# Kernel tuning notes

Measured on AMD Instinct MI355X. Metric: run time of the kernel, lower is better.

The kernel has to match this reference:

```python
import jax, jax.numpy as jnp
import numpy as np

DEPTH = 10
NUM_LEAVES = 2 ** DEPTH  # 1024


def setup_inputs() -> dict:
    key = jax.random.key(0)
    k1, k2, k3, k4 = jax.random.split(key, 4)
    B, C, T = 4096, 512, 4096
    x = jax.random.normal(k1, (B, C), dtype=jnp.float32)
    # thresholds = 6*rand - 3, as in __init__
    thresholds = 6.0 * jax.random.uniform(k2, (T, NUM_LEAVES - 1), dtype=jnp.float32) - 3.0
    ordinals = jax.random.randint(k3, (T, NUM_LEAVES - 1), 0, C, dtype=jnp.int32)
    weights = jax.random.normal(k4, (T, NUM_LEAVES), dtype=jnp.float32)
    return {"x": x, "thresholds": thresholds, "ordinals": ordinals, "weights": weights}


def reference(x, thresholds, ordinals, weights):
    """Random hinge forest forward.

    For each sample b and tree t: traverse the perfect binary tree of depth
    DEPTH.  At node n, margin m = x[b, ordinals[t, n]] - thresholds[t, n];
    go right (child 2n+2) if m > 0 else left (child 2n+1).  Track the signed
    margin of minimum magnitude along the path.  Output is
    |min-margin| * weights[t, leaf].
    """
    B = x.shape[0]
    T = thresholds.shape[0]
    tr = jnp.arange(T)  # [T], broadcasts against [B, T] node indices
    node = jnp.zeros((B, T), dtype=jnp.int32)
    minm = jnp.full((B, T), jnp.inf, dtype=x.dtype)
    for _ in range(DEPTH):
        thr = thresholds[tr, node]                      # [B, T]
        ordv = ordinals[tr, node]                       # [B, T] feature ids
        feat = jnp.take_along_axis(x, ordv, axis=1)     # [B, T]
        m = feat - thr
        minm = jnp.where(jnp.abs(m) < jnp.abs(minm), m, minm)
        node = 2 * node + 1 + (m > 0).astype(jnp.int32)
    leaf = node - (NUM_LEAVES - 1)                      # [B, T] in [0, 2^depth)
    w = weights[tr, leaf]                               # [B, T]
    return jnp.abs(minm) * w
```

## Files before the change

kernel.cpp:

```cpp
#include <hip/hip_runtime.h>
#include <hip/hip_fp16.h>

#define BB 4096
#define CC 512
#define TT 4096
#define NN 1023
#define NL 1024
#define DEPTH 10


__device__ __forceinline__ unsigned pack_node(float th, int o) {
    return ((unsigned)o << 16) | (unsigned)__half_as_ushort(__float2half(th));
}

__global__ __launch_bounds__(256)
void pack_trees(const float* __restrict__ thr, const int* __restrict__ ord,
                const float* __restrict__ wts,
                unsigned* __restrict__ pk_lo, uint4* __restrict__ tails) {
    int t = blockIdx.x, tid = threadIdx.x;
    const float* tr = thr + (size_t)t * NN;
    const int*   oo = ord + (size_t)t * NN;
    unsigned* plo = pk_lo + ((size_t)t << 9);
    #pragma unroll
    for (int k = 0; k < 2; ++k) {
        int j = k * 256 + tid;
        plo[j] = (j == 0) ? 0u : pack_node(tr[j - 1], oo[j - 1]);
    }
    int i = tid;
    int nL = 511 + 2 * i, nR = 512 + 2 * i;
    unsigned ndL = pack_node(tr[nL], oo[nL]);
    unsigned ndR = pack_node(tr[nR], oo[nR]);
    float4 w4 = *(const float4*)(wts + ((size_t)t << 10) + 4 * i);
    unsigned w01 = (unsigned)__half_as_ushort(__float2half(w4.x)) |
                   ((unsigned)__half_as_ushort(__float2half(w4.y)) << 16);
    unsigned w23 = (unsigned)__half_as_ushort(__float2half(w4.z)) |
                   ((unsigned)__half_as_ushort(__float2half(w4.w)) << 16);
    tails[((size_t)t << 8) + i] = make_uint4(ndL, ndR, w01, w23);
}

__global__ __launch_bounds__(256)
void pack_x16(const float* __restrict__ x, unsigned short* __restrict__ xt16) {
    __shared__ float tile[64][65];
    int tx = threadIdx.x & 63, ty = threadIdx.x >> 6;
    int b0 = blockIdx.x * 64;
    int c0 = blockIdx.y * 64;
    #pragma unroll
    for (int i = 0; i < 16; ++i) {
        int rr = i * 4 + ty;
        tile[rr][tx] = x[(size_t)(b0 + rr) * CC + c0 + tx];
    }
    __syncthreads();
    #pragma unroll
    for (int i = 0; i < 16; ++i) {
        int cr = i * 4 + ty;
        xt16[(size_t)(c0 + cr) * BB + b0 + tx] =
            __half_as_ushort(__float2half(tile[tx][cr]));
    }
}

#define LDS_BYTES 163840

typedef __attribute__((address_space(1))) const void gv_t;
typedef __attribute__((address_space(3))) void lv_t;

__global__ __launch_bounds__(1024, 1)
void rhf_main(const unsigned* __restrict__ pk_lo, const uint4* __restrict__ tails,
              const unsigned short* __restrict__ xt16, float* __restrict__ out) {
    extern __shared__ char smem[];
    unsigned short* xs16 = (unsigned short*)smem;
    unsigned*       trl  = (unsigned*)(smem + 65536);
    float*          res  = (float*)(smem + 131072);

    const int tid  = threadIdx.x;
    const int lane = tid & 63;
    const int wv   = tid >> 6;
    const int bi   = blockIdx.x;
    const int tb    = ((bi & 7) << 2) + ((bi >> 3) >> 6);
    const int panel = (bi >> 3) & 63;

    const char* gsrc0 = (const char*)pk_lo + ((size_t)(tb * 128) << 11);
    char* ldst = (char*)trl + wv * 4096 + lane * 16;
    auto dma = [&](int g) {
        const char* s = gsrc0 + ((size_t)(g * 32 + wv * 2) << 11) + lane * 16;
        #pragma unroll
        for (int q = 0; q < 4; ++q)
            __builtin_amdgcn_global_load_lds((gv_t*)(s + q * 1024),
                                             (lv_t*)(ldst + q * 1024), 16, 0, 0);
    };

    dma(0);

    {
        const unsigned short* src = xt16 + (size_t)panel * 64;
        #pragma unroll
        for (int k = 0; k < 4; ++k) {
            int i4 = k * 1024 + tid;
            int c  = i4 >> 3;
            int o8 = (i4 & 7) << 3;
            uint4 v = *(const uint4*)(src + (size_t)c * BB + o8);
            *(uint4*)(xs16 + ((size_t)i4 << 3)) = v;
        }
    }
    __syncthreads();

    #pragma unroll 1
    for (int g = 0; g < 4; ++g) {
        if (g > 0) {
            asm volatile("s_waitcnt vmcnt(0)" ::: "memory");
            __builtin_amdgcn_sched_barrier(0);
        }
        const int t0 = tb * 128 + g * 32 + wv * 2;
        const unsigned* pkw = trl + wv * 1024;

        float amin[2]; int sl[2]; unsigned nd[2]; uint4 rec[2];
        #pragma unroll
        for (int c = 0; c < 2; ++c) {
            amin[c] = __builtin_inff(); sl[c] = 1; nd[c] = pkw[c * 512 + 1];
        }

        #pragma unroll
        for (int d = 0; d < 9; ++d) {
            uint2 ch[2];
            #pragma unroll
            for (int c = 0; c < 2; ++c) {
                if (d < 8) ch[c] = *(const uint2*)(pkw + c * 512 + 2 * sl[c]);
                else       rec[c] = tails[((size_t)(t0 + c) << 8) + (sl[c] - 256)];
            }
            #pragma unroll
            for (int c = 0; c < 2; ++c) {
                float thv = __half2float(__ushort_as_half((unsigned short)(nd[c] & 0xffffu)));
                int   orv = (int)(nd[c] >> 16);
                float feat = __half2float(__ushort_as_half(xs16[(orv << 6) + lane]));
                float m = feat - thv;
                amin[c] = fminf(amin[c], fabsf(m));
                int right = (m > 0.0f) ? 1 : 0;
                sl[c] = 2 * sl[c] + right;
                if (d < 8) nd[c] = right ? ch[c].y : ch[c].x;
            }
        }

        if (g < 3) { dma(g + 1); __builtin_amdgcn_sched_barrier(0); }

        #pragma unroll
        for (int c = 0; c < 2; ++c) {
            int right8 = sl[c] & 1;
            unsigned nd9 = right8 ? rec[c].y : rec[c].x;
            float thv = __half2float(__ushort_as_half((unsigned short)(nd9 & 0xffffu)));
            int   orv = (int)(nd9 >> 16);
            float feat = __half2float(__ushort_as_half(xs16[(orv << 6) + lane]));
            float m = feat - thv;
            amin[c] = fminf(amin[c], fabsf(m));
            int right9 = (m > 0.0f) ? 1 : 0;
            unsigned wsel = right8 ? rec[c].w : rec[c].z;
            unsigned short wb = (unsigned short)(right9 ? (wsel >> 16) : (wsel & 0xffffu));
            float w = __half2float(__ushort_as_half(wb));
            int col = g * 32 + wv * 2 + c;
            res[(lane << 7) + ((col + lane) & 127)] = amin[c] * w;
        }
    }
    __syncthreads();

    float* obase = out + (size_t)(tb * 128);
    #pragma unroll
    for (int k = 0; k < 8; ++k) {
        int idx = k * 1024 + tid;
        int rr = idx >> 7, cc = idx & 127;
        float v = res[(rr << 7) + ((cc + rr) & 127)];
        obase[((size_t)panel * 64 + rr) * TT + cc] = v;
    }
}

#define F_SP 32
#define F_TG 16
#define F_GROUPS 8
#define F_TPB (F_TG * F_GROUPS)
#define F_NPANELS (BB / F_SP)
#define F_LDS 147456

__global__ __launch_bounds__(512, 1)
void rhf_fallback(const float* __restrict__ x, const float* __restrict__ thr_g,
                  const int* __restrict__ ord_g, const float* __restrict__ wts,
                  float* __restrict__ out) {
    extern __shared__ char smem[];
    float*        xs  = (float*)(smem);
    unsigned int* pk  = (unsigned int*)(smem + 65536);
    float*        res = (float*)(smem + 131072);
    const int tid = threadIdx.x, s = tid & 31, slot = tid >> 5;
    const int panel = blockIdx.x & (F_NPANELS - 1), tb = blockIdx.x >> 7;
    const float* xbase = x + (size_t)panel * F_SP * CC;
    #pragma unroll
    for (int k = 0; k < (F_SP * CC) / 512; ++k) {
        int idx = k * 512 + tid, r = idx >> 9, c = idx & 511;
        xs[(c << 5) + r] = xbase[r * CC + c];
    }
    float4 pthr[8]; int4 pord[8]; float tthr[3]; int tord[3];
    auto prefetch = [&](int g) {
        const size_t base = (size_t)(tb * F_TPB + g * F_TG + slot) * NN;
        #pragma unroll
        for (int k = 0; k < 8; ++k) {
            int j = k * 128 + 4 * s;
            if (j < 1020) { pthr[k] = *(const float4*)(thr_g + base + j);
                            pord[k] = *(const int4*)(ord_g + base + j); }
            else { tthr[0]=thr_g[base+1020]; tord[0]=ord_g[base+1020];
                   tthr[1]=thr_g[base+1021]; tord[1]=ord_g[base+1021];
                   tthr[2]=thr_g[base+1022]; tord[2]=ord_g[base+1022]; }
        }
    };
    auto pack1 = [](float f, int o) -> unsigned int {
        return ((unsigned int)o << 16) | (unsigned int)__half_as_ushort(__float2half(f));
    };
    auto commit = [&]() {
        unsigned int* pt = pk + (slot << 10);
        #pragma unroll
        for (int k = 0; k < 8; ++k) {
            int j = k * 128 + 4 * s;
            if (j < 1020) {
                pt[1+j+0]=pack1(pthr[k].x,pord[k].x); pt[1+j+1]=pack1(pthr[k].y,pord[k].y);
                pt[1+j+2]=pack1(pthr[k].z,pord[k].z); pt[1+j+3]=pack1(pthr[k].w,pord[k].w);
            } else { pt[1+1020]=pack1(tthr[0],tord[0]); pt[1+1021]=pack1(tthr[1],tord[1]);
                     pt[1+1022]=pack1(tthr[2],tord[2]); }
        }
    };
    prefetch(0);
    __builtin_amdgcn_sched_barrier(0);
    for (int g = 0; g < F_GROUPS; ++g) {
        __syncthreads();
        commit();
        __syncthreads();
        if (g + 1 < F_GROUPS) prefetch(g + 1);
        __builtin_amdgcn_sched_barrier(0);
        const int t = tb * F_TPB + g * F_TG + slot;
        const unsigned int* pkt = pk + (slot << 10);
        float minm = __builtin_inff();
        int sl = 1;
        unsigned int cur = pkt[1];
        #pragma unroll
        for (int d = 0; d < DEPTH; ++d) {
            uint2 ch;
            if (d < DEPTH - 1) ch = *(const uint2*)(pkt + 2 * sl);
            float thv = __half2float(__ushort_as_half((unsigned short)(cur & 0xffffu)));
            int orv = (int)(cur >> 16);
            float feat = xs[(orv << 5) + s];
            float m = feat - thv;
            bool take = fabsf(m) < fabsf(minm);
            minm = take ? m : minm;
            int right = (m > 0.0f) ? 1 : 0;
            sl = 2 * sl + right;
            if (d < DEPTH - 1) cur = right ? ch.y : ch.x;
        }
        int leaf = sl - NL;
        float w = wts[(size_t)t * NL + leaf];
        int col = g * F_TG + slot;
        res[(s << 7) + ((col + s) & 127)] = fabsf(minm) * w;
    }
    __syncthreads();
    float* obase = out + (size_t)panel * F_SP * TT + (size_t)tb * F_TPB;
    #pragma unroll
    for (int k = 0; k < (F_SP * F_TPB) / 512; ++k) {
        int idx = k * 512 + tid, rr = idx >> 7, c = idx & 127;
        obase[(size_t)rr * TT + c] = res[(rr << 7) + ((c + rr) & 127)];
    }
}

extern "C" void kernel_launch(void* const* d_in, const int* in_sizes, int n_in,
                              void* d_out, int out_size, void* d_ws, size_t ws_size,
                              hipStream_t stream) {
    const float* x    = (const float*)d_in[0];
    const float* thr  = (const float*)d_in[1];
    const int*   ordv = (const int*)d_in[2];
    const float* wts  = (const float*)d_in[3];
    float*       out  = (float*)d_out;

    const size_t pk_bytes   = (size_t)TT * 512 * 4;
    const size_t tail_bytes = (size_t)TT * 256 * 16;
    const size_t xt_bytes   = (size_t)CC * BB * 2;

    if (d_ws && ws_size >= pk_bytes + tail_bytes + xt_bytes) {
        unsigned*       pk_lo = (unsigned*)d_ws;
        uint4*          tails = (uint4*)((char*)d_ws + pk_bytes);
        unsigned short* xt16  = (unsigned short*)((char*)d_ws + pk_bytes + tail_bytes);
        pack_trees<<<TT, 256, 0, stream>>>(thr, ordv, wts, pk_lo, tails);
        dim3 gx(BB / 64, CC / 64);
        pack_x16<<<gx, 256, 0, stream>>>(x, xt16);
        hipFuncSetAttribute((const void*)rhf_main,
                            hipFuncAttributeMaxDynamicSharedMemorySize, LDS_BYTES);
        rhf_main<<<2048, 1024, LDS_BYTES, stream>>>(pk_lo, tails, xt16, out);
    } else {
        hipFuncSetAttribute((const void*)rhf_fallback,
                            hipFuncAttributeMaxDynamicSharedMemorySize, F_LDS);
        rhf_fallback<<<F_NPANELS * (TT / F_TPB), 512, F_LDS, stream>>>(x, thr, ordv, wts, out);
    }
}
```

Before: 114.5 us.

## Use packed fp16 margin math and prefetch tail records one level earlier

The per-node margin computation for the two trees each wave handles now runs as one packed f16x2 subtract. The running minimum is kept as a packed u16 min on the sign-cleared bits, replacing separate fp32 converts, subtracts and mins. The global tail-record loads are issued at depth 7 and fetch both candidate records, so their latency overlaps two traversal levels instead of one. The costs are twice the tail load traffic, and margins and the right/left decision now computed in fp16 rather than fp32, which can change rounding near zero and the minimum-magnitude value.

```diff
diff --git a/kernel.cpp b/kernel.cpp
--- a/kernel.cpp
+++ b/kernel.cpp
@@ -58,6 +58,29 @@
     }
 }
 
+typedef unsigned short u16x2 __attribute__((ext_vector_type(2)));
+
+static __device__ __forceinline__ unsigned psub_f16x2(unsigned a, unsigned b) {
+    __half2 ah, bh;
+    __builtin_memcpy(&ah, &a, 4);
+    __builtin_memcpy(&bh, &b, 4);
+    __half2 r = ah - bh;
+    unsigned u; __builtin_memcpy(&u, &r, 4); return u;
+}
+static __device__ __forceinline__ unsigned pmin_u16x2(unsigned a, unsigned b) {
+    u16x2 av, bv;
+    __builtin_memcpy(&av, &a, 4);
+    __builtin_memcpy(&bv, &b, 4);
+    u16x2 m = __builtin_elementwise_min(av, bv);
+    unsigned u; __builtin_memcpy(&u, &m, 4); return u;
+}
+static __device__ __forceinline__ float f16lo_to_f32(unsigned u) {
+    return __half2float(__ushort_as_half((unsigned short)(u & 0xffffu)));
+}
+static __device__ __forceinline__ float f16hi_to_f32(unsigned u) {
+    return __half2float(__ushort_as_half((unsigned short)(u >> 16)));
+}
+
 #define LDS_BYTES 163840
 
 typedef __attribute__((address_space(1))) const void gv_t;
@@ -112,51 +135,74 @@
         const int t0 = tb * 128 + g * 32 + wv * 2;
         const unsigned* pkw = trl + wv * 1024;
 
-        float amin[2]; int sl[2]; unsigned nd[2]; uint4 rec[2];
-        #pragma unroll
-        for (int c = 0; c < 2; ++c) {
-            amin[c] = __builtin_inff(); sl[c] = 1; nd[c] = pkw[c * 512 + 1];
-        }
+        unsigned amin2u = 0x7c007c00u;
+        int sl0 = 1, sl1 = 1;
+        unsigned nd0 = pkw[1], nd1 = pkw[512 + 1];
+        uint4 recL0, recR0, recL1, recR1;
 
         #pragma unroll
         for (int d = 0; d < 9; ++d) {
-            uint2 ch[2];
-            #pragma unroll
-            for (int c = 0; c < 2; ++c) {
-                if (d < 8) ch[c] = *(const uint2*)(pkw + c * 512 + 2 * sl[c]);
-                else       rec[c] = tails[((size_t)(t0 + c) << 8) + (sl[c] - 256)];
+            uint2 ch0, ch1;
+            if (d < 8) {
+                ch0 = *(const uint2*)(pkw + 2 * sl0);
+                ch1 = *(const uint2*)(pkw + 512 + 2 * sl1);
             }
-            #pragma unroll
-            for (int c = 0; c < 2; ++c) {
-                float thv = __half2float(__ushort_as_half((unsigned short)(nd[c] & 0xffffu)));
-                int   orv = (int)(nd[c] >> 16);
-                float feat = __half2float(__ushort_as_half(xs16[(orv << 6) + lane]));
-                float m = feat - thv;
-                amin[c] = fminf(amin[c], fabsf(m));
-                int right = (m > 0.0f) ? 1 : 0;
-                sl[c] = 2 * sl[c] + right;
-                if (d < 8) nd[c] = right ? ch[c].y : ch[c].x;
+            if (d == 7) {
+                const uint4* tp0 = tails + ((size_t)t0 << 8) + 2 * (sl0 - 128);
+                const uint4* tp1 = tails + ((size_t)(t0 + 1) << 8) + 2 * (sl1 - 128);
+                recL0 = tp0[0]; recR0 = tp0[1];
+                recL1 = tp1[0]; recR1 = tp1[1];
             }
+            unsigned thv2  = (nd0 & 0xffffu) | (nd1 << 16);
+            unsigned short f0 = xs16[((nd0 >> 16) << 6) + lane];
+            unsigned short f1 = xs16[((nd1 >> 16) << 6) + lane];
+            unsigned feat2 = (unsigned)f0 | ((unsigned)f1 << 16);
+            unsigned mb = psub_f16x2(feat2, thv2);
+            amin2u = pmin_u16x2(amin2u, mb & 0x7fff7fffu);
+            unsigned r0 = ((mb >> 15) & 1u) ^ 1u;
+            unsigned r1 = (mb >> 31) ^ 1u;
+            sl0 = 2 * sl0 + (int)r0;
+            sl1 = 2 * sl1 + (int)r1;
+            if (d < 8) {
+                nd0 = r0 ? ch0.y : ch0.x;
+                nd1 = r1 ? ch1.y : ch1.x;
+            }
         }
 
         if (g < 3) { dma(g + 1); __builtin_amdgcn_sched_barrier(0); }
 
-        #pragma unroll
-        for (int c = 0; c < 2; ++c) {
-            int right8 = sl[c] & 1;
-            unsigned nd9 = right8 ? rec[c].y : rec[c].x;
-            float thv = __half2float(__ushort_as_half((unsigned short)(nd9 & 0xffffu)));
-            int   orv = (int)(nd9 >> 16);
-            float feat = __half2float(__ushort_as_half(xs16[(orv << 6) + lane]));
-            float m = feat - thv;
-            amin[c] = fminf(amin[c], fabsf(m));
-            int right9 = (m > 0.0f) ? 1 : 0;
-            unsigned wsel = right8 ? rec[c].w : rec[c].z;
-            unsigned short wb = (unsigned short)(right9 ? (wsel >> 16) : (wsel & 0xffffu));
-            float w = __half2float(__ushort_as_half(wb));
-            int col = g * 32 + wv * 2 + c;
-            res[(lane << 7) + ((col + lane) & 127)] = amin[c] * w;
-        }
+        int r7_0 = (sl0 >> 1) & 1, r8_0 = sl0 & 1;
+        int r7_1 = (sl1 >> 1) & 1, r8_1 = sl1 & 1;
+        unsigned ndA0 = r8_0 ? recL0.y : recL0.x;
+        unsigned ndB0 = r8_0 ? recR0.y : recR0.x;
+        unsigned nd9_0 = r7_0 ? ndB0 : ndA0;
+        unsigned ndA1 = r8_1 ? recL1.y : recL1.x;
+        unsigned ndB1 = r8_1 ? recR1.y : recR1.x;
+        unsigned nd9_1 = r7_1 ? ndB1 : ndA1;
+
+        unsigned thv2  = (nd9_0 & 0xffffu) | (nd9_1 << 16);
+        unsigned short f0 = xs16[((nd9_0 >> 16) << 6) + lane];
+        unsigned short f1 = xs16[((nd9_1 >> 16) << 6) + lane];
+        unsigned feat2 = (unsigned)f0 | ((unsigned)f1 << 16);
+        unsigned mb = psub_f16x2(feat2, thv2);
+        amin2u = pmin_u16x2(amin2u, mb & 0x7fff7fffu);
+        unsigned r9_0 = ((mb >> 15) & 1u) ^ 1u;
+        unsigned r9_1 = (mb >> 31) ^ 1u;
+
+        unsigned wA0 = r8_0 ? recL0.w : recL0.z;
+        unsigned wB0 = r8_0 ? recR0.w : recR0.z;
+        unsigned ws0 = r7_0 ? wB0 : wA0;
+        unsigned short wb0 = (unsigned short)(r9_0 ? (ws0 >> 16) : (ws0 & 0xffffu));
+        unsigned wA1 = r8_1 ? recL1.w : recL1.z;
+        unsigned wB1 = r8_1 ? recR1.w : recR1.z;
+        unsigned ws1 = r7_1 ? wB1 : wA1;
+        unsigned short wb1 = (unsigned short)(r9_1 ? (ws1 >> 16) : (ws1 & 0xffffu));
+
+        float o0 = f16lo_to_f32(amin2u) * __half2float(__ushort_as_half(wb0));
+        float o1 = f16hi_to_f32(amin2u) * __half2float(__ushort_as_half(wb1));
+        int col0 = g * 32 + wv * 2;
+        res[(lane << 7) + ((col0 + lane) & 127)]     = o0;
+        res[(lane << 7) + ((col0 + 1 + lane) & 127)] = o1;
     }
     __syncthreads();
 
@@ -282,11 +328,11 @@
         pack_trees<<<TT, 256, 0, stream>>>(thr, ordv, wts, pk_lo, tails);
         dim3 gx(BB / 64, CC / 64);
         pack_x16<<<gx, 256, 0, stream>>>(x, xt16);
-        hipFuncSetAttribute((const void*)rhf_main,
+        (void)hipFuncSetAttribute((const void*)rhf_main,
                             hipFuncAttributeMaxDynamicSharedMemorySize, LDS_BYTES);
         rhf_main<<<2048, 1024, LDS_BYTES, stream>>>(pk_lo, tails, xt16, out);
     } else {
-        hipFuncSetAttribute((const void*)rhf_fallback,
+        (void)hipFuncSetAttribute((const void*)rhf_fallback,
                             hipFuncAttributeMaxDynamicSharedMemorySize, F_LDS);
         rhf_fallback<<<F_NPANELS * (TT / F_TPB), 512, F_LDS, stream>>>(x, thr, ordv, wts, out);
     }
```

Result: slower. 119.1 us (+4.1%).
